# Kernel optimization log

Measured on AMD Instinct MI355X. Metric: run time of the kernel, lower is better.

Reference implementation:

```python
import math
import jax, jax.numpy as jnp
from jax import lax
import numpy as np

B, H_IMG, W_IMG = 16, 512, 512
POOL, RATIO, SCALE = 23, 2, 0.25

def conv2d(x, w, b=None, stride=1, pad=0):
    y = lax.conv_general_dilated(x, w, (stride, stride), [(pad, pad), (pad, pad)],
                                 dimension_numbers=('NCHW', 'OIHW', 'NCHW'))
    return y if b is None else y + b[None, :, None, None]

def batchnorm(x, g, b, eps=1e-5):
    # training-mode BN (module is never put in eval mode): batch statistics
    m = x.mean((0, 2, 3), keepdims=True)
    v = x.var((0, 2, 3), keepdims=True)
    return g[None, :, None, None] * (x - m) * lax.rsqrt(v + eps) + b[None, :, None, None]

def maxpool(x, k, s, p=0):
    return lax.reduce_window(x, -jnp.inf, lax.max, (1, 1, k, k), (1, 1, s, s),
                             [(0, 0), (0, 0), (p, p), (p, p)])

def affine_grid(theta, H, W):
    # F.affine_grid, align_corners=False
    xs = (jnp.arange(W, dtype=jnp.float32) * 2 + 1) / W - 1
    ys = (jnp.arange(H, dtype=jnp.float32) * 2 + 1) / H - 1
    gx, gy = jnp.meshgrid(xs, ys)  # [H,W]
    base = jnp.stack([gx, gy, jnp.ones_like(gx)], axis=-1)  # [H,W,3]
    return base @ theta.T  # [H,W,2] -> (x,y) source coords

def grid_sample(imgs, grid):
    # bilinear, zero padding, align_corners=False; imgs [B,C,H,W], grid [H,W,2]
    _, C, H, W = imgs.shape
    ix = ((grid[..., 0] + 1) * W - 1) * 0.5
    iy = ((grid[..., 1] + 1) * H - 1) * 0.5
    x0, y0 = jnp.floor(ix), jnp.floor(iy)
    wa = (x0 + 1 - ix) * (y0 + 1 - iy)
    wb = (x0 + 1 - ix) * (iy - y0)
    wc = (ix - x0) * (y0 + 1 - iy)
    wd = (ix - x0) * (iy - y0)
    def gather(img, yy, xx):
        valid = (xx >= 0) & (xx < W) & (yy >= 0) & (yy < H)
        return img[:, jnp.clip(yy, 0, H - 1).astype(jnp.int32),
                      jnp.clip(xx, 0, W - 1).astype(jnp.int32)] * valid
    def one(img):
        return (gather(img, y0, x0) * wa + gather(img, y0 + 1, x0) * wb +
                gather(img, y0, x0 + 1) * wc + gather(img, y0 + 1, x0 + 1) * wd)
    return jax.vmap(one)(imgs)

def roialign(feat, ind, boxes):
    # torchvision ROIAlign(output=(23,23), spatial_scale=0.25, sampling_ratio=2, aligned=False)
    C, H, W = feat.shape[1:]
    x1, y1, x2, y2 = (boxes * SCALE).T
    bw = jnp.maximum(x2 - x1, 1.0) / POOL
    bh = jnp.maximum(y2 - y1, 1.0) / POOL
    off = (jnp.arange(RATIO, dtype=jnp.float32) + 0.5) / RATIO
    pos = (jnp.arange(POOL, dtype=jnp.float32)[:, None] + off[None, :]).reshape(-1)  # [46]
    ys = y1[:, None] + pos[None, :] * bh[:, None]  # [N,46]
    xs = x1[:, None] + pos[None, :] * bw[:, None]
    S = POOL * RATIO
    def one(img, yv, xv):
        empty = ((yv[:, None] < -1.0) | (yv[:, None] > H) |
                 (xv[None, :] < -1.0) | (xv[None, :] > W))  # [S,S]
        y = jnp.broadcast_to(jnp.clip(yv, 0.0, H - 1.0)[:, None], (S, S))
        x = jnp.broadcast_to(jnp.clip(xv, 0.0, W - 1.0)[None, :], (S, S))
        y0f, x0f = jnp.floor(y), jnp.floor(x)
        y0 = y0f.astype(jnp.int32); x0 = x0f.astype(jnp.int32)
        y1i = jnp.minimum(y0 + 1, H - 1); x1i = jnp.minimum(x0 + 1, W - 1)
        ly, lx = y - y0f, x - x0f
        hy, hx = 1.0 - ly, 1.0 - lx
        v = (img[:, y0, x0] * (hy * hx) + img[:, y0, x1i] * (hy * lx) +
             img[:, y1i, x0] * (ly * hx) + img[:, y1i, x1i] * (ly * lx))
        v = jnp.where(empty[None], 0.0, v)
        return v.reshape(C, POOL, RATIO, POOL, RATIO).mean((2, 4))
    return jax.vmap(one)(feat[ind], ys, xs)  # [N,C,23,23]

def forward(x, box, stem_w, stem_g, stem_b, conv1_w, conv1_b, bn1_g, bn1_b,
            conv2_w, conv2_b, fc1_w, fc1_b, head_w, head_b):
    x = x.transpose(0, 3, 1, 2)  # NHWC -> NCHW
    # resnet stem (7x7/2 conv + BN + ReLU + 3x3/2 maxpool): 64 ch @ stride 4
    f = maxpool(jax.nn.relu(batchnorm(conv2d(x, stem_w, stride=2, pad=3), stem_g, stem_b)), 3, 2, 1)
    Bc, C, H, W = f.shape
    a = -5 * math.pi / 180
    theta1 = jnp.array([[math.cos(a), math.sin(-a), 0.0], [math.sin(a), math.cos(a), 0.0]], jnp.float32)
    a = 5 * math.pi / 180
    theta2 = jnp.array([[math.cos(a), math.sin(-a), 0.0], [math.sin(a), math.cos(a), 0.0]], jnp.float32)
    xt1 = grid_sample(f, affine_grid(theta1, H, W))
    xt2 = grid_sample(f, affine_grid(theta2, H, W))
    ind = jnp.arange(Bc, dtype=jnp.int32)
    b7 = box.reshape(Bc, 7, 4)
    # focus1..focus7 on f, channel order matches torch.cat((f1..f7), dim=1)
    boxes7 = b7.transpose(1, 0, 2).reshape(7 * Bc, 4)
    f7 = roialign(f, jnp.tile(ind, 7), boxes7).reshape(7, Bc, C, POOL, POOL)
    f7 = f7.transpose(1, 0, 2, 3, 4).reshape(Bc, 7 * C, POOL, POOL)
    b1, b2 = b7[:, 0], b7[:, 1]
    f8 = roialign(xt1, ind, b1)
    f9 = roialign(xt1, ind, b2)
    f10 = roialign(xt2, ind, b1)
    f11 = roialign(xt2, ind, b2)
    h = jnp.concatenate([f7, f8, f9, f10, f11], axis=1)  # [B,704,23,23]
    h = maxpool(jax.nn.relu(batchnorm(conv2d(h, conv1_w, conv1_b), bn1_g, bn1_b)), 2, 2)  # [B,64,10,10]
    h = jax.nn.relu(conv2d(h, conv2_w, conv2_b))  # [B,32,8,8]
    h = h.reshape(Bc, 32 * 8 * 8)
    h = jax.nn.relu(h @ fc1_w.T + fc1_b)
    return jnp.tanh(h @ head_w.T + head_b)  # [B,12]

def setup_inputs() -> dict:
    key = jax.random.key(0)
    ks = jax.random.split(key, 8)
    x = jax.random.normal(ks[0], (B, H_IMG, W_IMG, 3), jnp.float32)
    xy = jax.random.uniform(ks[1], (B, 7, 2), jnp.float32, 0.0, 300.0)
    wh = jax.random.uniform(ks[2], (B, 7, 2), jnp.float32, 50.0, 200.0)
    box = jnp.concatenate([xy, xy + wh], axis=-1).reshape(B, 28)
    def w(k, shape, fan_in):
        return jax.random.normal(k, shape, jnp.float32) / np.float32(np.sqrt(fan_in))
    return dict(
        x=x, box=box,
        stem_w=w(ks[3], (64, 3, 7, 7), 3 * 49),
        stem_g=jnp.ones((64,), jnp.float32), stem_b=jnp.zeros((64,), jnp.float32),
        conv1_w=w(ks[4], (64, 704, 3, 3), 704 * 9), conv1_b=jnp.zeros((64,), jnp.float32),
        bn1_g=jnp.ones((64,), jnp.float32), bn1_b=jnp.zeros((64,), jnp.float32),
        conv2_w=w(ks[5], (32, 64, 3, 3), 64 * 9), conv2_b=jnp.zeros((32,), jnp.float32),
        fc1_w=w(ks[6], (128, 2048), 2048), fc1_b=jnp.zeros((128,), jnp.float32),
        head_w=w(ks[7], (12, 128), 128), head_b=jnp.zeros((12,), jnp.float32),
    )

def reference(x, box, stem_w, stem_g, stem_b, conv1_w, conv1_b, bn1_g, bn1_b,
              conv2_w, conv2_b, fc1_w, fc1_b, head_w, head_b):
    return forward(x, box, stem_w, stem_g, stem_b, conv1_w, conv1_b, bn1_g, bn1_b,
                   conv2_w, conv2_b, fc1_w, fc1_b, head_w, head_b)
```

## Files before the change

### kernel.cpp

```cpp
#include <hip/hip_runtime.h>
#include <hip/hip_bf16.h>


#define C5 0.9961946980917455f
#define S5 0.08715574274765817f

typedef __attribute__((ext_vector_type(8))) short short8;
typedef __attribute__((ext_vector_type(4))) float f32x4;

typedef __attribute__((address_space(3))) ushort lds_ushort;
typedef const __attribute__((address_space(1))) ushort gbl_ushort;

__device__ __forceinline__ ushort f2bf_bits(float v) {
    __hip_bfloat16 b = __float2bfloat16(v);
    ushort u;
    __builtin_memcpy(&u, &b, 2);
    return u;
}
__device__ __forceinline__ float bfbits2f(ushort u) {
    __hip_bfloat16 b;
    __builtin_memcpy(&b, &u, 2);
    return __bfloat162float(b);
}

__global__ __launch_bounds__(256) void k_cvt(const float* __restrict__ w1,
                                             __hip_bfloat16* __restrict__ w1b,
                                             const float* __restrict__ sw,
                                             __hip_bfloat16* __restrict__ w2b,
                                             float* __restrict__ stats_raw) {
    const int t = blockIdx.x * 256 + threadIdx.x;
    if (t < 405504) {
        w1b[t] = __float2bfloat16(w1[t]);
    } else if (t < 417792) {
        const int e = t - 405504;
        const int oc = e / 192, k = e - oc * 192;
        const int kh = k / 24, u = k - kh * 24;
        float v = 0.f;
        if (u >= 3 && kh < 7) {
            int tt = u - 3;
            int kw = tt / 3, ci = tt - kw * 3;
            v = sw[oc * 147 + ci * 49 + kh * 7 + kw];
        }
        w2b[e] = __float2bfloat16(v);
    } else if (t < 417920) {
        stats_raw[t - 417792] = 0.f;
    }
}

__global__ __launch_bounds__(256) void k_cvtx(const float* __restrict__ x,
                                              ushort* __restrict__ xbf) {
    const int t = blockIdx.x * 256 + threadIdx.x;
    if (t >= 3232480) return;
    const int n = t / 202020;
    const int r = t - n * 202020;
    const int row = r / 390, col = r - row * 390;
    const int ih = row - 3;
    float4 v = {0.f, 0.f, 0.f, 0.f};
    if ((unsigned)ih < 512u && col >= 3 && col <= 386)
        v = *(const float4*)(x + (size_t)n * 786432 + (size_t)ih * 1536 + 4 * col - 12);
    uint2 p;
    p.x = (uint)f2bf_bits(v.x) | ((uint)f2bf_bits(v.y) << 16);
    p.y = (uint)f2bf_bits(v.z) | ((uint)f2bf_bits(v.w) << 16);
    *(uint2*)(xbf + 4 * (size_t)t) = p;
}

__global__ __launch_bounds__(64, 4) void k_stem(const ushort* __restrict__ xbf,
                                                const ushort* __restrict__ w2b,
                                                __hip_bfloat16* __restrict__ out) {
    __shared__ __align__(16) ushort lds[4608];
    const int bx = blockIdx.x;
    const int gi = ((bx & 7) << 11) + (bx >> 3);
    const int wq = gi & 3;
    const int oh = (gi >> 2) & 255;
    const int n  = gi >> 10;
    const int lane = threadIdx.x;
    const int quad = lane >> 4, m = lane & 15;
    const int p0 = wq * 64;

    {
        const ushort* src = xbf + (size_t)n * 808080 + (size_t)(oh * 2) * 1560 + 6 * p0;
        if (lane < 51) {
#pragma unroll
            for (int row = 0; row < 8; row++)
                __builtin_amdgcn_global_load_lds((gbl_ushort*)(src + row * 1560 + lane * 8),
                                                 (lds_ushort*)(lds + row * 416 + lane * 8),
                                                 16, 0, 0);
        }
    }
    asm volatile("s_waitcnt vmcnt(0)" ::: "memory");
    __builtin_amdgcn_sched_barrier(0);

    f32x4 acc[4][4] = {};
#pragma unroll
    for (int ks = 0; ks < 6; ks++) {
        const int g   = ks * 4 + quad;
        const int kh  = g / 3;
        const int gi2 = g - kh * 3;
        const uint* rr = (const uint*)lds + kh * 208 + 4 * gi2;
        short8 b[4];
#pragma unroll
        for (int nt = 0; nt < 4; nt++) {
            const uint* q = rr + 3 * (nt * 16 + m);
            uint4 t = (uint4){q[0], q[1], q[2], q[3]};
            __builtin_memcpy(&b[nt], &t, 16);
        }
        const int ko = ks * 32 + quad * 8;
#pragma unroll
        for (int mt = 0; mt < 4; mt++) {
            const short8 a = *(const short8*)(w2b + (size_t)(mt * 16 + m) * 192 + ko);
#pragma unroll
            for (int nt = 0; nt < 4; nt++)
                acc[mt][nt] = __builtin_amdgcn_mfma_f32_16x16x32_bf16(a, b[nt], acc[mt][nt], 0, 0, 0);
        }
    }

#pragma unroll
    for (int mt = 0; mt < 4; mt++)
#pragma unroll
        for (int nt = 0; nt < 4; nt++)
#pragma unroll
            for (int r = 0; r < 4; r++)
                lds[(mt * 16 + quad * 4 + r) * 72 + nt * 16 + m] = f2bf_bits(acc[mt][nt][r]);

    ushort* outb = (ushort*)out + (size_t)n * 64 * 65536 + oh * 256 + p0;
    const int ocl = lane >> 3, ch = lane & 7;
#pragma unroll
    for (int p = 0; p < 8; p++) {
        const int oc = p * 8 + ocl;
        uint4 v = *(const uint4*)&lds[oc * 72 + ch * 8];
        *(uint4*)(outb + (size_t)oc * 65536 + ch * 8) = v;
    }
}

__global__ __launch_bounds__(256) void k_sumstem(const ushort* __restrict__ stem,
                                                 float* __restrict__ stats_raw) {
    const int c = blockIdx.x >> 3, s = blockIdx.x & 7;
    const int tid = threadIdx.x;
    const uint4* b0 = (const uint4*)(stem + ((size_t)(s * 2) * 64 + c) * 65536);
    const uint4* b1 = (const uint4*)(stem + ((size_t)(s * 2 + 1) * 64 + c) * 65536);
    float sum = 0.f, sq = 0.f;
    for (int i = tid; i < 8192; i += 256) {
        uint4 v0 = b0[i], v1 = b1[i];
#pragma unroll
        for (int k = 0; k < 4; k++) {
            uint u0 = ((const uint*)&v0)[k], u1 = ((const uint*)&v1)[k];
            float a0 = __uint_as_float(u0 << 16);
            float a1 = __uint_as_float(u0 & 0xffff0000u);
            float a2 = __uint_as_float(u1 << 16);
            float a3 = __uint_as_float(u1 & 0xffff0000u);
            sum += a0 + a1 + a2 + a3;
            sq = fmaf(a0, a0, fmaf(a1, a1, fmaf(a2, a2, fmaf(a3, a3, sq))));
        }
    }
#pragma unroll
    for (int off = 32; off; off >>= 1) {
        sum += __shfl_xor(sum, off, 64);
        sq  += __shfl_xor(sq, off, 64);
    }
    __shared__ float shS[4], shQ[4];
    if ((tid & 63) == 0) { shS[tid >> 6] = sum; shQ[tid >> 6] = sq; }
    __syncthreads();
    if (tid == 0) {
        atomicAdd(&stats_raw[c * 2],     shS[0] + shS[1] + shS[2] + shS[3]);
        atomicAdd(&stats_raw[c * 2 + 1], shQ[0] + shQ[1] + shQ[2] + shQ[3]);
    }
}

__global__ __launch_bounds__(256) void k_bn1stats(const float* __restrict__ c1,
                                                  const float* __restrict__ gamma,
                                                  const float* __restrict__ beta,
                                                  float* __restrict__ stats1) {
    const int c = blockIdx.x;
    const int tid = threadIdx.x;
    float s = 0.f, ss = 0.f;
    for (int e = tid; e < 7056; e += 256) {
        int n = e / 441, p = e - n * 441;
        float v = c1[(n * 64 + c) * 441 + p];
        s += v; ss += v * v;
    }
    __shared__ float sh[8], sh2[8];
#pragma unroll
    for (int off = 32; off; off >>= 1) {
        s += __shfl_xor(s, off, 64);
        ss += __shfl_xor(ss, off, 64);
    }
    if ((tid & 63) == 0) { sh[tid >> 6] = s; sh2[tid >> 6] = ss; }
    __syncthreads();
    if (tid == 0) {
        s = sh[0] + sh[1] + sh[2] + sh[3];
        ss = sh2[0] + sh2[1] + sh2[2] + sh2[3];
        const float inv_n = 1.f / 7056.f;
        float mn = s * inv_n;
        float var = ss * inv_n - mn * mn;
        float a = gamma[c] * rsqrtf(var + 1e-5f);
        stats1[c] = a;
        stats1[64 + c] = beta[c] - mn * a;
    }
}

__global__ __launch_bounds__(256) void k_bnpool(const __hip_bfloat16* __restrict__ sin_,
                                                const float* __restrict__ stats_raw,
                                                const float* __restrict__ gamma,
                                                const float* __restrict__ beta,
                                                float* __restrict__ f) {
    const int idx = blockIdx.x * 256 + threadIdx.x;
    const int pwg = idx & 15;
    const int ph = (idx >> 4) & 127;
    const int c = (idx >> 11) & 63;
    const int n = idx >> 17;
    const int pw0 = pwg * 8;
    const float inv_n = 1.f / 1048576.f;
    const float S = stats_raw[c * 2], Q = stats_raw[c * 2 + 1];
    const float mn = S * inv_n;
    const float var = Q * inv_n - mn * mn;
    const float a = gamma[c] * rsqrtf(var + 1e-5f);
    const float b = beta[c] - mn * a;
    const uint* base = (const uint*)((const ushort*)sin_ + (size_t)(n * 64 + c) * 65536);

    float colmax[17];
#pragma unroll
    for (int k = 0; k < 17; k++) colmax[k] = -1e30f;

    const int r0 = ph * 2 - 1;
#pragma unroll
    for (int dr = 0; dr < 3; dr++) {
        const int r = r0 + dr;
        const bool rv = (unsigned)r < 256u;
        uint d[9];
        const uint* rp = base + r * 128 + pw0 - 1;
#pragma unroll
        for (int j = 0; j < 9; j++)
            d[j] = (rv && (pw0 > 0 || j > 0)) ? rp[j] : 0u;
#pragma unroll
        for (int j = 0; j < 9; j++) {
            float vhi = a * bfbits2f((ushort)(d[j] >> 16)) + b;
            colmax[2 * j] = rv ? fmaxf(colmax[2 * j], vhi) : colmax[2 * j];
            if (j > 0) {
                float vlo = a * bfbits2f((ushort)(d[j] & 0xFFFFu)) + b;
                colmax[2 * j - 1] = rv ? fmaxf(colmax[2 * j - 1], vlo) : colmax[2 * j - 1];
            }
        }
    }
    if (pw0 == 0) colmax[0] = -1e30f;

    float o[8];
#pragma unroll
    for (int i = 0; i < 8; i++)
        o[i] = fmaxf(fmaxf(colmax[2 * i], fmaxf(colmax[2 * i + 1], colmax[2 * i + 2])), 0.f);
    float* fp = f + (size_t)(n * 64 + c) * 16384 + ph * 128 + pw0;
    *(float4*)fp       = (float4){o[0], o[1], o[2], o[3]};
    *(float4*)(fp + 4) = (float4){o[4], o[5], o[6], o[7]};
}

__device__ __forceinline__ float gs_pad(const float* band, int ry0g,
                                        float ix, float iy) {
    float x0f = floorf(ix), y0f = floorf(iy);
    float lx = ix - x0f, ly = iy - y0f;
    float hx = 1.f - lx, hy = 1.f - ly;
    const int base = ((int)y0f - ry0g) * 144 + (int)x0f + 8;
    return band[base] * (hx * hy) + band[base + 144] * (hx * ly)
         + band[base + 1] * (lx * hy) + band[base + 145] * (lx * ly);
}

__global__ __launch_bounds__(256, 3) void k_gridsample2(const float* __restrict__ f,
                                                        float* __restrict__ xt1,
                                                        float* __restrict__ xt2) {
    __shared__ float band[78 * 144];
    const int bx = blockIdx.x;
    const int half = bx & 1;
    const int img_i = bx >> 1;
    const int h0 = half * 64;
    const int ry0g = half ? 57 : -7;
    const float* img = f + (size_t)img_i * 16384;
    const int tid = threadIdx.x;
    for (int e = tid; e < 78 * 36; e += 256) {
        const int r = e / 36, q = e - r * 36;
        const int gr = ry0g + r;
        float4 v = {0.f, 0.f, 0.f, 0.f};
        if ((unsigned)gr < 128u && q >= 2 && q <= 33)
            v = *(const float4*)(img + gr * 128 + 4 * q - 8);
        ((float4*)band)[e] = v;
    }
    __syncthreads();

    float* o1 = xt1 + (size_t)img_i * 16384 + h0 * 128;
    float* o2 = xt2 + (size_t)img_i * 16384 + h0 * 128;
    for (int e = tid; e < 8192; e += 256) {
        const int h = h0 + (e >> 7);
        const int w = e & 127;
        float gx = (2 * w + 1) * (1.f / 128.f) - 1.f;
        float gy = (2 * h + 1) * (1.f / 128.f) - 1.f;
        float g0a = C5 * gx + S5 * gy,  g1a = -S5 * gx + C5 * gy;
        float g0b = C5 * gx - S5 * gy,  g1b =  S5 * gx + C5 * gy;
        o1[e] = gs_pad(band, ry0g, ((g0a + 1.f) * 128.f - 1.f) * 0.5f,
                                   ((g1a + 1.f) * 128.f - 1.f) * 0.5f);
        o2[e] = gs_pad(band, ry0g, ((g0b + 1.f) * 128.f - 1.f) * 0.5f,
                                   ((g1b + 1.f) * 128.f - 1.f) * 0.5f);
    }
}

__global__ __launch_bounds__(256) void k_roialign(const float* __restrict__ f,
                                                  const float* __restrict__ xt1,
                                                  const float* __restrict__ xt2,
                                                  const float* __restrict__ box,
                                                  __hip_bfloat16* __restrict__ h) {
    __shared__ float reg[52 * 53];
    const int bx = blockIdx.x;
    const int job = bx % 11;
    const int nc = bx / 11;
    const int c = nc & 63;
    const int n = nc >> 6;
    int j, cbase;
    const float* src;
    if (job < 7)      { j = job;     cbase = job * 64;             src = f;   }
    else if (job < 9) { j = job - 7; cbase = 448 + (job - 7) * 64; src = xt1; }
    else              { j = job - 9; cbase = 576 + (job - 9) * 64; src = xt2; }
    const float* bp = box + n * 28 + j * 4;
    const float x1 = bp[0] * 0.25f, y1 = bp[1] * 0.25f;
    const float x2 = bp[2] * 0.25f, y2 = bp[3] * 0.25f;
    const float bw = fmaxf(x2 - x1, 1.f) * (1.f / 23.f);
    const float bh = fmaxf(y2 - y1, 1.f) * (1.f / 23.f);

    const int ry0 = (int)floorf(fminf(fmaxf(y1 + 0.25f * bh, 0.f), 127.f));
    int ry1 = min((int)floorf(fminf(fmaxf(y1 + 22.75f * bh, 0.f), 127.f)) + 1, 127);
    ry1 = min(ry1, ry0 + 51);
    const int rx0 = (int)floorf(fminf(fmaxf(x1 + 0.25f * bw, 0.f), 127.f));
    int rx1 = min((int)floorf(fminf(fmaxf(x1 + 22.75f * bw, 0.f), 127.f)) + 1, 127);
    rx1 = min(rx1, rx0 + 51);
    const int RH = ry1 - ry0 + 1, RW = rx1 - rx0 + 1;

    const float* img = src + (size_t)(n * 64 + c) * 16384;
    const int tid = threadIdx.x;
    const int lane = tid & 63, wv = tid >> 6;
    for (int r = wv; r < RH; r += 4)
        if (lane < RW)
            reg[r * 53 + lane] = img[(ry0 + r) * 128 + rx0 + lane];
    __syncthreads();

    __hip_bfloat16* hb = h + (size_t)(n * 704 + cbase + c) * 529;
    for (int pp = tid; pp < 529; pp += 256) {
        const int ph = pp / 23, pw = pp - ph * 23;
        float sum = 0.f;
#pragma unroll
        for (int s = 0; s < 4; s++) {
            const int r1 = s >> 1, r2 = s & 1;
            const float yv = y1 + (ph + r1 * 0.5f + 0.25f) * bh;
            const float xv = x1 + (pw + r2 * 0.5f + 0.25f) * bw;
            const bool ok = !(yv < -1.f || yv > 128.f || xv < -1.f || xv > 128.f);
            float y = fminf(fmaxf(yv, 0.f), 127.f);
            float x = fminf(fmaxf(xv, 0.f), 127.f);
            float y0f = floorf(y), x0f = floorf(x);
            int y0 = (int)y0f, x0 = (int)x0f;
            int iy0 = y0 - ry0, ix0 = x0 - rx0;
            int iy1 = min(y0 + 1, 127) - ry0, ix1 = min(x0 + 1, 127) - rx0;
            float ly = y - y0f, lx = x - x0f;
            float hy = 1.f - ly, hx = 1.f - lx;
            const float sc = ok ? 1.f : 0.f;
            sum += sc * (reg[iy0 * 53 + ix0] * (hy * hx) + reg[iy0 * 53 + ix1] * (hy * lx)
                       + reg[iy1 * 53 + ix0] * (ly * hx) + reg[iy1 * 53 + ix1] * (ly * lx));
        }
        hb[pp] = __float2bfloat16(sum * 0.25f);
    }
}

__global__ __launch_bounds__(256) void k_conv1m(const ushort* __restrict__ hb,
                                                const ushort* __restrict__ w1b,
                                                float* __restrict__ c1p) {
    __shared__ __align__(16) ushort Bs[2][2][32][40];
    const int bx = blockIdx.x;
    const int pt = bx % 17;
    const int n  = (bx / 17) & 15;
    const int s  = bx / 272;
    const int tid = threadIdx.x;
    const int w = tid >> 6, lane = tid & 63;
    const int quad = lane >> 4, m = lane & 15;
    const int kbase = s * 2112;
    const int posb = pt * 32;
    const size_t hb_n = (size_t)n * 704 * 529;
    f32x4 acc0 = {0.f, 0.f, 0.f, 0.f};
    f32x4 acc1 = {0.f, 0.f, 0.f, 0.f};
    const ushort* wrow = w1b + (size_t)(w * 16 + m) * 6336;

    int ep[8], ek[8], epos[8];
#pragma unroll
    for (int i = 0; i < 8; i++) {
        const int e = tid + 256 * i;
        ep[i] = e >> 10; ek[i] = (e >> 5) & 31; epos[i] = e & 31;
    }
    ushort rbuf[8];
#pragma unroll
    for (int i = 0; i < 8; i++) {
        const int k = kbase + ep[i] * 32 + ek[i];
        const int ci = k / 9, tap = k - ci * 9;
        const int kh = tap / 3, kw = tap - kh * 3;
        rbuf[i] = hb[hb_n + (size_t)ci * 529 + kh * 23 + kw + posb + epos[i]];
    }
#pragma unroll
    for (int i = 0; i < 8; i++) Bs[0][ep[i]][epos[i]][ek[i]] = rbuf[i];

    for (int it = 0; it < 33; it++) {
        __syncthreads();
        const int cur = it & 1;
        if (it < 32) {
            const int k0 = kbase + (it + 1) * 64;
#pragma unroll
            for (int i = 0; i < 8; i++) {
                const int k = k0 + ep[i] * 32 + ek[i];
                const int ci = k / 9, tap = k - ci * 9;
                const int kh = tap / 3, kw = tap - kh * 3;
                rbuf[i] = hb[hb_n + (size_t)ci * 529 + kh * 23 + kw + posb + epos[i]];
            }
        }
        const int k0 = kbase + it * 64;
        const short8 a0  = *(const short8*)(wrow + k0 + quad * 8);
        const short8 a1  = *(const short8*)(wrow + k0 + 32 + quad * 8);
        const short8 b00 = *(const short8*)&Bs[cur][0][m][quad * 8];
        const short8 b01 = *(const short8*)&Bs[cur][0][16 + m][quad * 8];
        const short8 b10 = *(const short8*)&Bs[cur][1][m][quad * 8];
        const short8 b11 = *(const short8*)&Bs[cur][1][16 + m][quad * 8];
        acc0 = __builtin_amdgcn_mfma_f32_16x16x32_bf16(a0, b00, acc0, 0, 0, 0);
        acc1 = __builtin_amdgcn_mfma_f32_16x16x32_bf16(a0, b01, acc1, 0, 0, 0);
        acc0 = __builtin_amdgcn_mfma_f32_16x16x32_bf16(a1, b10, acc0, 0, 0, 0);
        acc1 = __builtin_amdgcn_mfma_f32_16x16x32_bf16(a1, b11, acc1, 0, 0, 0);
        if (it < 32) {
#pragma unroll
            for (int i = 0; i < 8; i++) Bs[cur ^ 1][ep[i]][epos[i]][ek[i]] = rbuf[i];
        }
    }
    float* outp = c1p + ((size_t)(s * 16 + n) * 64) * 544;
#pragma unroll
    for (int r = 0; r < 4; r++) {
        const int oc = w * 16 + quad * 4 + r;
        outp[(size_t)oc * 544 + posb + m]      = acc0[r];
        outp[(size_t)oc * 544 + posb + 16 + m] = acc1[r];
    }
}

__global__ __launch_bounds__(256) void k_c1red(const float* __restrict__ c1p,
                                               const float* __restrict__ b1,
                                               float* __restrict__ c1) {
    const int t = blockIdx.x * 256 + threadIdx.x;
    const int p = t % 441;
    const int oc = (t / 441) % 64;
    const int n = t / 28224;
    const int ph = p / 21, pw = p - ph * 21;
    const int p529 = ph * 23 + pw;
    const size_t base = ((size_t)n * 64 + oc) * 544 + p529;
    const size_t sstr = (size_t)16 * 64 * 544;
    c1[t] = c1p[base] + c1p[base + sstr] + c1p[base + 2 * sstr] + b1[oc];
}

__global__ __launch_bounds__(256) void k_bnpool2(const float* __restrict__ c1,
                                                 const float* __restrict__ stats1,
                                                 float* __restrict__ p1) {
    const int t = blockIdx.x * 256 + threadIdx.x;
    const int pw = t % 10;
    const int ph = (t / 10) % 10;
    const int c = (t / 100) % 64;
    const int n = t / 6400;
    const float a = stats1[c], b = stats1[64 + c];
    const float* base = c1 + (size_t)(n * 64 + c) * 441;
    const int r = ph * 2, cc = pw * 2;
    float v0 = a * base[r * 21 + cc] + b;
    float v1 = a * base[r * 21 + cc + 1] + b;
    float v2 = a * base[(r + 1) * 21 + cc] + b;
    float v3 = a * base[(r + 1) * 21 + cc + 1] + b;
    p1[t] = fmaxf(fmaxf(fmaxf(v0, v1), fmaxf(v2, v3)), 0.f);
}

__global__ __launch_bounds__(256) void k_conv2(const float* __restrict__ p1,
                                               const float* __restrict__ w2,
                                               const float* __restrict__ b2,
                                               float* __restrict__ c2) {
    __shared__ float ip[6400];
    __shared__ float wl[2304];
    const int bx = blockIdx.x;
    const int n = bx >> 3, ocq = bx & 7;
    const int tid = threadIdx.x;
    const float4* p14 = (const float4*)(p1 + (size_t)n * 6400);
    float4* ip4 = (float4*)ip;
    for (int e = tid; e < 1600; e += 256) ip4[e] = p14[e];
    for (int e = tid; e < 2304; e += 256) wl[e] = w2[ocq * 2304 + e];
    __syncthreads();

    const int ocl = tid >> 6, pos = tid & 63;
    const int ph = pos >> 3, pw = pos & 7;
    const int oc = ocq * 4 + ocl;
    float s = b2[oc];
    const float* wb = wl + ocl * 576;
    const float* ib = ip + ph * 10 + pw;
    for (int ci = 0; ci < 64; ci++) {
        const float* r = ib + ci * 100;
        const float* ww = wb + ci * 9;
        s += r[0] * ww[0] + r[1] * ww[1] + r[2] * ww[2]
           + r[10] * ww[3] + r[11] * ww[4] + r[12] * ww[5]
           + r[20] * ww[6] + r[21] * ww[7] + r[22] * ww[8];
    }
    c2[(size_t)(n * 32 + oc) * 64 + pos] = fmaxf(s, 0.f);
}

__global__ __launch_bounds__(64) void k_fc1(const float* __restrict__ c2,
                                            const float* __restrict__ fw,
                                            const float* __restrict__ fb,
                                            float* __restrict__ fo) {
    const int bx = blockIdx.x;
    const int oc = bx & 127, n = bx >> 7;
    const int lane = threadIdx.x;
    const float* a = c2 + (size_t)n * 2048;
    const float* w = fw + (size_t)oc * 2048;
    float s = 0.f;
    for (int k = lane; k < 2048; k += 64) s += a[k] * w[k];
#pragma unroll
    for (int off = 32; off; off >>= 1) s += __shfl_xor(s, off, 64);
    if (lane == 0) fo[n * 128 + oc] = fmaxf(s + fb[oc], 0.f);
}

__global__ __launch_bounds__(64) void k_head(const float* __restrict__ fo,
                                             const float* __restrict__ hw,
                                             const float* __restrict__ hb,
                                             float* __restrict__ out) {
    const int bx = blockIdx.x;
    const int oc = bx % 12, n = bx / 12;
    const int lane = threadIdx.x;
    float s = 0.f;
    for (int k = lane; k < 128; k += 64) s += fo[n * 128 + k] * hw[oc * 128 + k];
#pragma unroll
    for (int off = 32; off; off >>= 1) s += __shfl_xor(s, off, 64);
    if (lane == 0) out[bx] = tanhf(s + hb[oc]);
}

extern "C" void kernel_launch(void* const* d_in, const int* in_sizes, int n_in,
                              void* d_out, int out_size, void* d_ws, size_t ws_size,
                              hipStream_t stream) {
    const float* x       = (const float*)d_in[0];
    const float* box     = (const float*)d_in[1];
    const float* stem_w  = (const float*)d_in[2];
    const float* stem_g  = (const float*)d_in[3];
    const float* stem_b  = (const float*)d_in[4];
    const float* conv1_w = (const float*)d_in[5];
    const float* conv1_b = (const float*)d_in[6];
    const float* bn1_g   = (const float*)d_in[7];
    const float* bn1_b   = (const float*)d_in[8];
    const float* conv2_w = (const float*)d_in[9];
    const float* conv2_b = (const float*)d_in[10];
    const float* fc1_w   = (const float*)d_in[11];
    const float* fc1_b   = (const float*)d_in[12];
    const float* head_w  = (const float*)d_in[13];
    const float* head_b  = (const float*)d_in[14];
    float* out = (float*)d_out;
    float* w = (float*)d_ws;

    const size_t F_SZ = 16777216;
    float* f   = w;
    ushort* xbf = (ushort*)w;
    __hip_bfloat16* stem = (__hip_bfloat16*)(w + F_SZ);
    float* xt1 = w + F_SZ;
    float* xt2 = w + 2 * F_SZ;
    float* base3 = w + 3 * F_SZ;
    __hip_bfloat16* hbuf = (__hip_bfloat16*)base3;
    float* c1   = base3 + 2979392;
    float* c1p  = c1 + 451584;
    float* p1   = c1p + 1671168;
    float* c2   = p1 + 102400;
    float* fo   = c2 + 32768;
    float* stats_raw = fo + 2048;
    float* stats1  = stats_raw + 128;
    __hip_bfloat16* w1b = (__hip_bfloat16*)(stats1 + 128);
    __hip_bfloat16* w2b = (__hip_bfloat16*)(stats1 + 128 + 202752);

    k_cvt<<<1633, 256, 0, stream>>>(conv1_w, w1b, stem_w, w2b, stats_raw);
    k_cvtx<<<12627, 256, 0, stream>>>(x, xbf);
    k_stem<<<16384, 64, 0, stream>>>(xbf, (const ushort*)w2b, stem);
    k_sumstem<<<512, 256, 0, stream>>>((const ushort*)stem, stats_raw);
    k_bnpool<<<8192, 256, 0, stream>>>(stem, stats_raw, stem_g, stem_b, f);
    k_gridsample2<<<2048, 256, 0, stream>>>(f, xt1, xt2);
    k_roialign<<<11264, 256, 0, stream>>>(f, xt1, xt2, box, hbuf);
    k_conv1m<<<816, 256, 0, stream>>>((const ushort*)hbuf, (const ushort*)w1b, c1p);
    k_c1red<<<1764, 256, 0, stream>>>(c1p, conv1_b, c1);
    k_bn1stats<<<64, 256, 0, stream>>>(c1, bn1_g, bn1_b, stats1);
    k_bnpool2<<<400, 256, 0, stream>>>(c1, stats1, p1);
    k_conv2<<<128, 256, 0, stream>>>(p1, conv2_w, conv2_b, c2);
    k_fc1<<<2048, 64, 0, stream>>>(c2, fc1_w, fc1_b, fo);
    k_head<<<192, 64, 0, stream>>>(fo, head_w, head_b, out);
}
```

Before: 430.0 us.

## Fuse stem BN statistics into stem GEMM, merge conversion kernels, widen conv1 split-K

The stem kernel now reduces per-channel sums and sums of squares from its fp32 accumulators and atomically adds them into eight striped partial buffers. This removes the separate k_sumstem pass that re-read the full bf16 stem output. The weight and input conversion kernels are merged into one launch, and conv1's split-K factor goes from 3 to 9 slices, with c1p relocated into the big workspace region and the reduce kernel summing nine partials. The trade-off is many atomics from 16384 blocks and slightly different statistics, since they are now taken from fp32 values rather than rounded bf16.

```diff
diff --git a/kernel.cpp b/kernel.cpp
--- a/kernel.cpp
+++ b/kernel.cpp
@@ -23,51 +23,54 @@
     return __bfloat162float(b);
 }
 
-__global__ __launch_bounds__(256) void k_cvt(const float* __restrict__ w1,
-                                             __hip_bfloat16* __restrict__ w1b,
-                                             const float* __restrict__ sw,
-                                             __hip_bfloat16* __restrict__ w2b,
-                                             float* __restrict__ stats_raw) {
-    const int t = blockIdx.x * 256 + threadIdx.x;
-    if (t < 405504) {
-        w1b[t] = __float2bfloat16(w1[t]);
-    } else if (t < 417792) {
-        const int e = t - 405504;
-        const int oc = e / 192, k = e - oc * 192;
-        const int kh = k / 24, u = k - kh * 24;
-        float v = 0.f;
-        if (u >= 3 && kh < 7) {
-            int tt = u - 3;
-            int kw = tt / 3, ci = tt - kw * 3;
-            v = sw[oc * 147 + ci * 49 + kh * 7 + kw];
-        }
-        w2b[e] = __float2bfloat16(v);
-    } else if (t < 417920) {
-        stats_raw[t - 417792] = 0.f;
-    }
-}
-
-__global__ __launch_bounds__(256) void k_cvtx(const float* __restrict__ x,
-                                              ushort* __restrict__ xbf) {
-    const int t = blockIdx.x * 256 + threadIdx.x;
-    if (t >= 3232480) return;
-    const int n = t / 202020;
-    const int r = t - n * 202020;
-    const int row = r / 390, col = r - row * 390;
-    const int ih = row - 3;
-    float4 v = {0.f, 0.f, 0.f, 0.f};
-    if ((unsigned)ih < 512u && col >= 3 && col <= 386)
-        v = *(const float4*)(x + (size_t)n * 786432 + (size_t)ih * 1536 + 4 * col - 12);
-    uint2 p;
-    p.x = (uint)f2bf_bits(v.x) | ((uint)f2bf_bits(v.y) << 16);
-    p.y = (uint)f2bf_bits(v.z) | ((uint)f2bf_bits(v.w) << 16);
-    *(uint2*)(xbf + 4 * (size_t)t) = p;
+__global__ __launch_bounds__(256) void k_cvtall(const float* __restrict__ x,
+                                                ushort* __restrict__ xbf,
+                                                const float* __restrict__ w1,
+                                                __hip_bfloat16* __restrict__ w1b,
+                                                const float* __restrict__ sw,
+                                                __hip_bfloat16* __restrict__ w2b,
+                                                float* __restrict__ partial) {
+    const int bx = blockIdx.x;
+    if (bx < 12627) {
+        const int t = bx * 256 + threadIdx.x;
+        if (t >= 3232480) return;
+        const int n = t / 202020;
+        const int r = t - n * 202020;
+        const int row = r / 390, col = r - row * 390;
+        const int ih = row - 3;
+        float4 v = {0.f, 0.f, 0.f, 0.f};
+        if ((unsigned)ih < 512u && col >= 3 && col <= 386)
+            v = *(const float4*)(x + (size_t)n * 786432 + (size_t)ih * 1536 + 4 * col - 12);
+        uint2 p;
+        p.x = (uint)f2bf_bits(v.x) | ((uint)f2bf_bits(v.y) << 16);
+        p.y = (uint)f2bf_bits(v.z) | ((uint)f2bf_bits(v.w) << 16);
+        *(uint2*)(xbf + 4 * (size_t)t) = p;
+    } else {
+        const int t = (bx - 12627) * 256 + threadIdx.x;
+        if (t < 405504) {
+            w1b[t] = __float2bfloat16(w1[t]);
+        } else if (t < 417792) {
+            const int e = t - 405504;
+            const int oc = e / 192, k = e - oc * 192;
+            const int kh = k / 24, u = k - kh * 24;
+            float v = 0.f;
+            if (u >= 3 && kh < 7) {
+                int tt = u - 3;
+                int kw = tt / 3, ci = tt - kw * 3;
+                v = sw[oc * 147 + ci * 49 + kh * 7 + kw];
+            }
+            w2b[e] = __float2bfloat16(v);
+        } else if (t < 418816) {
+            partial[t - 417792] = 0.f;
+        }
+    }
 }
 
 __global__ __launch_bounds__(64, 4) void k_stem(const ushort* __restrict__ xbf,
                                                 const ushort* __restrict__ w2b,
-                                                __hip_bfloat16* __restrict__ out) {
-    __shared__ __align__(16) ushort lds[4608];
+                                                __hip_bfloat16* __restrict__ out,
+                                                float* __restrict__ partial) {
+    __shared__ __align__(16) ushort lds[4864];
     const int bx = blockIdx.x;
     const int gi = ((bx & 7) << 11) + (bx >> 3);
     const int wq = gi & 3;
@@ -76,6 +79,7 @@
     const int lane = threadIdx.x;
     const int quad = lane >> 4, m = lane & 15;
     const int p0 = wq * 64;
+    float2* sred = (float2*)(lds + 4608);
 
     {
         const ushort* src = xbf + (size_t)n * 808080 + (size_t)(oh * 2) * 1560 + 6 * p0;
@@ -115,6 +119,23 @@
     }
 
 #pragma unroll
+    for (int mt = 0; mt < 4; mt++) {
+#pragma unroll
+        for (int r = 0; r < 4; r++) {
+            float s = acc[mt][0][r] + acc[mt][1][r] + acc[mt][2][r] + acc[mt][3][r];
+            float q = acc[mt][0][r] * acc[mt][0][r] + acc[mt][1][r] * acc[mt][1][r]
+                    + acc[mt][2][r] * acc[mt][2][r] + acc[mt][3][r] * acc[mt][3][r];
+#pragma unroll
+            for (int off = 1; off < 16; off <<= 1) {
+                s += __shfl_xor(s, off, 64);
+                q += __shfl_xor(q, off, 64);
+            }
+            if (m == 0)
+                sred[mt * 16 + quad * 4 + r] = (float2){s, q};
+        }
+    }
+
+#pragma unroll
     for (int mt = 0; mt < 4; mt++)
 #pragma unroll
         for (int nt = 0; nt < 4; nt++)
@@ -130,39 +151,12 @@
         uint4 v = *(const uint4*)&lds[oc * 72 + ch * 8];
         *(uint4*)(outb + (size_t)oc * 65536 + ch * 8) = v;
     }
-}
-
-__global__ __launch_bounds__(256) void k_sumstem(const ushort* __restrict__ stem,
-                                                 float* __restrict__ stats_raw) {
-    const int c = blockIdx.x >> 3, s = blockIdx.x & 7;
-    const int tid = threadIdx.x;
-    const uint4* b0 = (const uint4*)(stem + ((size_t)(s * 2) * 64 + c) * 65536);
-    const uint4* b1 = (const uint4*)(stem + ((size_t)(s * 2 + 1) * 64 + c) * 65536);
-    float sum = 0.f, sq = 0.f;
-    for (int i = tid; i < 8192; i += 256) {
-        uint4 v0 = b0[i], v1 = b1[i];
-#pragma unroll
-        for (int k = 0; k < 4; k++) {
-            uint u0 = ((const uint*)&v0)[k], u1 = ((const uint*)&v1)[k];
-            float a0 = __uint_as_float(u0 << 16);
-            float a1 = __uint_as_float(u0 & 0xffff0000u);
-            float a2 = __uint_as_float(u1 << 16);
-            float a3 = __uint_as_float(u1 & 0xffff0000u);
-            sum += a0 + a1 + a2 + a3;
-            sq = fmaf(a0, a0, fmaf(a1, a1, fmaf(a2, a2, fmaf(a3, a3, sq))));
-        }
-    }
-#pragma unroll
-    for (int off = 32; off; off >>= 1) {
-        sum += __shfl_xor(sum, off, 64);
-        sq  += __shfl_xor(sq, off, 64);
-    }
-    __shared__ float shS[4], shQ[4];
-    if ((tid & 63) == 0) { shS[tid >> 6] = sum; shQ[tid >> 6] = sq; }
-    __syncthreads();
-    if (tid == 0) {
-        atomicAdd(&stats_raw[c * 2],     shS[0] + shS[1] + shS[2] + shS[3]);
-        atomicAdd(&stats_raw[c * 2 + 1], shQ[0] + shQ[1] + shQ[2] + shQ[3]);
+
+    {
+        float2 v = sred[lane];
+        float* pb = partial + ((bx & 7) << 7) + lane * 2;
+        atomicAdd(pb, v.x);
+        atomicAdd(pb + 1, v.y);
     }
 }
 
@@ -199,7 +193,7 @@
 }
 
 __global__ __launch_bounds__(256) void k_bnpool(const __hip_bfloat16* __restrict__ sin_,
-                                                const float* __restrict__ stats_raw,
+                                                const float* __restrict__ partial,
                                                 const float* __restrict__ gamma,
                                                 const float* __restrict__ beta,
                                                 float* __restrict__ f) {
@@ -209,8 +203,13 @@
     const int c = (idx >> 11) & 63;
     const int n = idx >> 17;
     const int pw0 = pwg * 8;
+    float S = 0.f, Q = 0.f;
+#pragma unroll
+    for (int rp = 0; rp < 8; rp++) {
+        S += partial[rp * 128 + c * 2];
+        Q += partial[rp * 128 + c * 2 + 1];
+    }
     const float inv_n = 1.f / 1048576.f;
-    const float S = stats_raw[c * 2], Q = stats_raw[c * 2 + 1];
     const float mn = S * inv_n;
     const float var = Q * inv_n - mn * mn;
     const float a = gamma[c] * rsqrtf(var + 1e-5f);
@@ -374,7 +373,7 @@
     const int tid = threadIdx.x;
     const int w = tid >> 6, lane = tid & 63;
     const int quad = lane >> 4, m = lane & 15;
-    const int kbase = s * 2112;
+    const int kbase = s * 704;
     const int posb = pt * 32;
     const size_t hb_n = (size_t)n * 704 * 529;
     f32x4 acc0 = {0.f, 0.f, 0.f, 0.f};
@@ -398,10 +397,10 @@
 #pragma unroll
     for (int i = 0; i < 8; i++) Bs[0][ep[i]][epos[i]][ek[i]] = rbuf[i];
 
-    for (int it = 0; it < 33; it++) {
+    for (int it = 0; it < 11; it++) {
         __syncthreads();
         const int cur = it & 1;
-        if (it < 32) {
+        if (it < 10) {
             const int k0 = kbase + (it + 1) * 64;
 #pragma unroll
             for (int i = 0; i < 8; i++) {
@@ -422,7 +421,7 @@
         acc1 = __builtin_amdgcn_mfma_f32_16x16x32_bf16(a0, b01, acc1, 0, 0, 0);
         acc0 = __builtin_amdgcn_mfma_f32_16x16x32_bf16(a1, b10, acc0, 0, 0, 0);
         acc1 = __builtin_amdgcn_mfma_f32_16x16x32_bf16(a1, b11, acc1, 0, 0, 0);
-        if (it < 32) {
+        if (it < 10) {
 #pragma unroll
             for (int i = 0; i < 8; i++) Bs[cur ^ 1][ep[i]][epos[i]][ek[i]] = rbuf[i];
         }
@@ -447,7 +446,10 @@
     const int p529 = ph * 23 + pw;
     const size_t base = ((size_t)n * 64 + oc) * 544 + p529;
     const size_t sstr = (size_t)16 * 64 * 544;
-    c1[t] = c1p[base] + c1p[base + sstr] + c1p[base + 2 * sstr] + b1[oc];
+    float v = 0.f;
+#pragma unroll
+    for (int k = 0; k < 9; k++) v += c1p[base + k * sstr];
+    c1[t] = v + b1[oc];
 }
 
 __global__ __launch_bounds__(256) void k_bnpool2(const float* __restrict__ c1,
@@ -553,29 +555,27 @@
     const size_t F_SZ = 16777216;
     float* f   = w;
     ushort* xbf = (ushort*)w;
+    float* c1p = w;
     __hip_bfloat16* stem = (__hip_bfloat16*)(w + F_SZ);
     float* xt1 = w + F_SZ;
     float* xt2 = w + 2 * F_SZ;
     float* base3 = w + 3 * F_SZ;
     __hip_bfloat16* hbuf = (__hip_bfloat16*)base3;
     float* c1   = base3 + 2979392;
-    float* c1p  = c1 + 451584;
-    float* p1   = c1p + 1671168;
+    float* p1   = c1 + 451584;
     float* c2   = p1 + 102400;
     float* fo   = c2 + 32768;
-    float* stats_raw = fo + 2048;
-    float* stats1  = stats_raw + 128;
+    float* partial = fo + 2048;
+    float* stats1  = partial + 1024;
     __hip_bfloat16* w1b = (__hip_bfloat16*)(stats1 + 128);
     __hip_bfloat16* w2b = (__hip_bfloat16*)(stats1 + 128 + 202752);
 
-    k_cvt<<<1633, 256, 0, stream>>>(conv1_w, w1b, stem_w, w2b, stats_raw);
-    k_cvtx<<<12627, 256, 0, stream>>>(x, xbf);
-    k_stem<<<16384, 64, 0, stream>>>(xbf, (const ushort*)w2b, stem);
-    k_sumstem<<<512, 256, 0, stream>>>((const ushort*)stem, stats_raw);
-    k_bnpool<<<8192, 256, 0, stream>>>(stem, stats_raw, stem_g, stem_b, f);
+    k_cvtall<<<14263, 256, 0, stream>>>(x, xbf, conv1_w, w1b, stem_w, w2b, partial);
+    k_stem<<<16384, 64, 0, stream>>>(xbf, (const ushort*)w2b, stem, partial);
+    k_bnpool<<<8192, 256, 0, stream>>>(stem, partial, stem_g, stem_b, f);
     k_gridsample2<<<2048, 256, 0, stream>>>(f, xt1, xt2);
     k_roialign<<<11264, 256, 0, stream>>>(f, xt1, xt2, box, hbuf);
-    k_conv1m<<<816, 256, 0, stream>>>((const ushort*)hbuf, (const ushort*)w1b, c1p);
+    k_conv1m<<<2448, 256, 0, stream>>>((const ushort*)hbuf, (const ushort*)w1b, c1p);
     k_c1red<<<1764, 256, 0, stream>>>(c1p, conv1_b, c1);
     k_bn1stats<<<64, 256, 0, stream>>>(c1, bn1_g, bn1_b, stats1);
     k_bnpool2<<<400, 256, 0, stream>>>(c1, stats1, p1);
```

New measurement: 507.7 us. 1.18x slower.
